# Optimization experiments

Hardware: AMD Instinct MI355X
Metric: run time of the kernel (lower is better)

Reference implementation:

```python
import jax, jax.numpy as jnp
import numpy as np


def setup_inputs() -> dict:
    key = jax.random.key(0)
    k1, k2 = jax.random.split(key)
    D0, D1, V = 64, 64, 25000
    # probability-like positive values (avoid log(0)); not normalized exactly,
    # matching how the loss only needs positive entries for log().
    p = jax.random.uniform(k1, (D0, D1, V), dtype=jnp.float32, minval=1e-4, maxval=1.0)
    q = jax.random.uniform(k2, (D0, D1, V), dtype=jnp.float32, minval=1e-4, maxval=1.0)
    p = p / jnp.sum(p, axis=-1, keepdims=True)
    q = q / jnp.sum(q, axis=-1, keepdims=True)
    return {"p_proba": p, "q_proba": q}


def reference(p_proba, q_proba):
    # mask[i, j] = 0 if argmax over vocab of p_proba[i, j] is index 0, else 1
    # (vectorized form of the original per-(i,j) python loop; original loops
    #  j over q_proba.size(0) which equals p_proba.size(1) here)
    mask = (jnp.argmax(p_proba, axis=-1) != 0).astype(p_proba.dtype)  # [D0, D1]
    mask = jax.lax.stop_gradient(mask)
    # elementwise KL term q * (log q - log p), masked and summed
    kl = q_proba * (jnp.log(q_proba) - jnp.log(p_proba))  # [D0, D1, V]
    masked_loss = jnp.sum(mask[:, :, None] * kl)
    return masked_loss / (p_proba.shape[1] * p_proba.shape[0])
```

## Files before the change

### kernel.cpp

```cpp
#include <hip/hip_runtime.h>


#define VOCAB   25000
#define VOCAB4  6250
#define BLOCK   256
#define BATCH   4
#define FULL_ITERS 6
#define LN2 0.69314718055994530942f

typedef float f4 __attribute__((ext_vector_type(4)));

__global__ __launch_bounds__(BLOCK) void kl_row_kernel(
    const float* __restrict__ p, const float* __restrict__ q,
    float* __restrict__ partial)
{
    const int row = blockIdx.x;
    const size_t base = (size_t)row * VOCAB;
    const f4* __restrict__ p4 = reinterpret_cast<const f4*>(p + base);
    const f4* __restrict__ q4 = reinterpret_cast<const f4*>(q + base);
    const int tid = threadIdx.x;

    float p0 = (tid == 0) ? p[base] : 0.0f;

    float s[BATCH]  = {0.f, 0.f, 0.f, 0.f};
    float mx[BATCH] = {-1.f, -1.f, -1.f, -1.f};

    int v = tid;
    for (int i = 0; i < FULL_ITERS; ++i, v += BATCH * BLOCK) {
        f4 P[BATCH], Q[BATCH];
        #pragma unroll
        for (int b = 0; b < BATCH; ++b) P[b] = p4[v + b * BLOCK];
        #pragma unroll
        for (int b = 0; b < BATCH; ++b) Q[b] = q4[v + b * BLOCK];

        #pragma unroll
        for (int b = 0; b < BATCH; ++b) {
            #pragma unroll
            for (int k = 0; k < 4; ++k)
                s[b] = fmaf(Q[b][k], __log2f(Q[b][k]) - __log2f(P[b][k]), s[b]);
            mx[b] = fmaxf(mx[b],
                     fmaxf(fmaxf(P[b][0], P[b][1]), fmaxf(P[b][2], P[b][3])));
        }
    }

    if (tid < (VOCAB4 - FULL_ITERS * BATCH * BLOCK)) {
        const int vr = FULL_ITERS * BATCH * BLOCK + tid;
        f4 P = p4[vr];
        f4 Q = q4[vr];
        #pragma unroll
        for (int k = 0; k < 4; ++k)
            s[0] = fmaf(Q[k], __log2f(Q[k]) - __log2f(P[k]), s[0]);
        mx[0] = fmaxf(mx[0], fmaxf(fmaxf(P[0], P[1]), fmaxf(P[2], P[3])));
    }

    float sum  = (s[0] + s[1]) + (s[2] + s[3]);
    float pmax = fmaxf(fmaxf(mx[0], mx[1]), fmaxf(mx[2], mx[3]));

    #pragma unroll
    for (int off = 32; off > 0; off >>= 1) {
        sum  += __shfl_down(sum, off, 64);
        pmax  = fmaxf(pmax, __shfl_down(pmax, off, 64));
    }

    __shared__ float ssum[BLOCK / 64];
    __shared__ float smax[BLOCK / 64];
    const int wave = tid >> 6;
    const int lane = tid & 63;
    if (lane == 0) { ssum[wave] = sum; smax[wave] = pmax; }
    __syncthreads();

    if (tid == 0) {
        float stot = (ssum[0] + ssum[1]) + (ssum[2] + ssum[3]);
        float m = fmaxf(fmaxf(smax[0], smax[1]), fmaxf(smax[2], smax[3]));
        partial[row] = (p0 < m) ? stot * LN2 : 0.0f;
    }
}

__global__ __launch_bounds__(BLOCK) void kl_final_reduce(
    const float* __restrict__ partial, int rows, float* __restrict__ out)
{
    const int tid = threadIdx.x;
    float sum = 0.0f;
    for (int i = tid; i < rows; i += BLOCK) sum += partial[i];

    #pragma unroll
    for (int off = 32; off > 0; off >>= 1)
        sum += __shfl_down(sum, off, 64);

    __shared__ float ssum[BLOCK / 64];
    const int wave = tid >> 6;
    const int lane = tid & 63;
    if (lane == 0) ssum[wave] = sum;
    __syncthreads();

    if (tid == 0) {
        float s = (ssum[0] + ssum[1]) + (ssum[2] + ssum[3]);
        out[0] = s / (float)rows;
    }
}

extern "C" void kernel_launch(void* const* d_in, const int* in_sizes, int n_in,
                              void* d_out, int out_size, void* d_ws, size_t ws_size,
                              hipStream_t stream)
{
    const float* p = (const float*)d_in[0];
    const float* q = (const float*)d_in[1];
    float* out = (float*)d_out;
    float* partial = (float*)d_ws;

    const int rows = in_sizes[0] / VOCAB;

    kl_row_kernel<<<rows, BLOCK, 0, stream>>>(p, q, partial);
    kl_final_reduce<<<1, BLOCK, 0, stream>>>(partial, rows, out);
}
```

Before: 750.9 us.

## Double-buffer row loads in registers and use nontemporal loads

Restructures the per-row loop into a software-pipelined ping-pong scheme. The next batch of p/q vectors is issued before the current batch is computed, and the remainder chunk is loaded up front, so more memory requests are in flight per thread. All loads become nontemporal to avoid polluting caches with streaming data. This doubles the live vector registers, which could lower occupancy.

```diff
diff --git a/kernel.cpp b/kernel.cpp
--- a/kernel.cpp
+++ b/kernel.cpp
@@ -5,10 +5,15 @@
 #define VOCAB4  6250
 #define BLOCK   256
 #define BATCH   4
+#define OFF     (BATCH * BLOCK)
 #define FULL_ITERS 6
+#define REM_BASE (FULL_ITERS * OFF)
+#define REM_CNT  (VOCAB4 - REM_BASE)
 #define LN2 0.69314718055994530942f
 
 typedef float f4 __attribute__((ext_vector_type(4)));
+
+#define NT(a) __builtin_nontemporal_load(a)
 
 __global__ __launch_bounds__(BLOCK) void kl_row_kernel(
     const float* __restrict__ p, const float* __restrict__ q,
@@ -25,32 +30,59 @@
     float s[BATCH]  = {0.f, 0.f, 0.f, 0.f};
     float mx[BATCH] = {-1.f, -1.f, -1.f, -1.f};
 
-    int v = tid;
-    for (int i = 0; i < FULL_ITERS; ++i, v += BATCH * BLOCK) {
-        f4 P[BATCH], Q[BATCH];
+    f4 Pa[BATCH], Qa[BATCH], Pb[BATCH], Qb[BATCH];
+    f4 Pr, Qr;
+    const bool hasrem = tid < REM_CNT;
+
+    #pragma unroll
+    for (int b = 0; b < BATCH; ++b) {
+        Pa[b] = NT(&p4[tid + b * BLOCK]);
+        Qa[b] = NT(&q4[tid + b * BLOCK]);
+    }
+    if (hasrem) {
+        Pr = NT(&p4[REM_BASE + tid]);
+        Qr = NT(&q4[REM_BASE + tid]);
+    }
+
+    #pragma unroll
+    for (int ii = 0; ii < FULL_ITERS / 2; ++ii) {
+        const int vB = tid + (2 * ii + 1) * OFF;
         #pragma unroll
-        for (int b = 0; b < BATCH; ++b) P[b] = p4[v + b * BLOCK];
-        #pragma unroll
-        for (int b = 0; b < BATCH; ++b) Q[b] = q4[v + b * BLOCK];
-
+        for (int b = 0; b < BATCH; ++b) {
+            Pb[b] = NT(&p4[vB + b * BLOCK]);
+            Qb[b] = NT(&q4[vB + b * BLOCK]);
+        }
         #pragma unroll
         for (int b = 0; b < BATCH; ++b) {
             #pragma unroll
             for (int k = 0; k < 4; ++k)
-                s[b] = fmaf(Q[b][k], __log2f(Q[b][k]) - __log2f(P[b][k]), s[b]);
+                s[b] = fmaf(Qa[b][k], __log2f(Qa[b][k]) - __log2f(Pa[b][k]), s[b]);
             mx[b] = fmaxf(mx[b],
-                     fmaxf(fmaxf(P[b][0], P[b][1]), fmaxf(P[b][2], P[b][3])));
+                     fmaxf(fmaxf(Pa[b][0], Pa[b][1]), fmaxf(Pa[b][2], Pa[b][3])));
+        }
+        if (ii + 1 < FULL_ITERS / 2) {
+            const int vA = tid + (2 * ii + 2) * OFF;
+            #pragma unroll
+            for (int b = 0; b < BATCH; ++b) {
+                Pa[b] = NT(&p4[vA + b * BLOCK]);
+                Qa[b] = NT(&q4[vA + b * BLOCK]);
+            }
+        }
+        #pragma unroll
+        for (int b = 0; b < BATCH; ++b) {
+            #pragma unroll
+            for (int k = 0; k < 4; ++k)
+                s[b] = fmaf(Qb[b][k], __log2f(Qb[b][k]) - __log2f(Pb[b][k]), s[b]);
+            mx[b] = fmaxf(mx[b],
+                     fmaxf(fmaxf(Pb[b][0], Pb[b][1]), fmaxf(Pb[b][2], Pb[b][3])));
         }
     }
 
-    if (tid < (VOCAB4 - FULL_ITERS * BATCH * BLOCK)) {
-        const int vr = FULL_ITERS * BATCH * BLOCK + tid;
-        f4 P = p4[vr];
-        f4 Q = q4[vr];
+    if (hasrem) {
         #pragma unroll
         for (int k = 0; k < 4; ++k)
-            s[0] = fmaf(Q[k], __log2f(Q[k]) - __log2f(P[k]), s[0]);
-        mx[0] = fmaxf(mx[0], fmaxf(fmaxf(P[0], P[1]), fmaxf(P[2], P[3])));
+            s[0] = fmaf(Qr[k], __log2f(Qr[k]) - __log2f(Pr[k]), s[0]);
+        mx[0] = fmaxf(mx[0], fmaxf(fmaxf(Pr[0], Pr[1]), fmaxf(Pr[2], Pr[3])));
     }
 
     float sum  = (s[0] + s[1]) + (s[2] + s[3]);
```

Measured after the change: 712.5 us. 1.05x faster.
